# Kernel tuning notes

Hardware: AMD Instinct MI355X
Metric: run time of the kernel (lower is better)

## Reference

```python
import jax, jax.numpy as jnp
import numpy as np

B, S, D, H, W = 2, 8192, 512, 8, 256   # batch, seq, d_model, heads, one-sided window
HD = D // H                            # head dim = 64
C = S // W                             # number of chunks of size W (seq % 2W == 0 holds)


def setup_inputs() -> dict:
    key = jax.random.key(0)
    ks = jax.random.split(key, 7)
    x = jax.random.normal(ks[0], (B, S, D), jnp.float32)
    def w(k):
        return jax.random.normal(k, (D, D), jnp.float32) * 0.02
    def b(k):
        return jax.random.normal(k, (D,), jnp.float32) * 0.02
    return {
        "x": x,
        "Wq": w(ks[1]), "bq": b(ks[2]),
        "Wk": w(ks[3]), "bk": b(ks[4]),
        "Wv": w(ks[5]), "bv": b(ks[6]),
    }


def _heads_chunked(t):
    # (B,S,D) -> (B*H, C, W, HD): split heads, then split sequence into chunks of W
    return t.reshape(B, S, H, HD).transpose(0, 2, 1, 3).reshape(B * H, C, W, HD)


def _three_chunks(t):
    # neighbor-chunk concat: for chunk c, gather chunks [c-1, c, c+1] (zero padded at ends)
    tp = jnp.pad(t, ((0, 0), (1, 1), (0, 0), (0, 0)))
    return jnp.concatenate([tp[:, :-2], tp[:, 1:-1], tp[:, 2:]], axis=2)  # (B*H, C, 3W, HD)


def reference(x, Wq, bq, Wk, bk, Wv, bv):
    scale = 1.0 / np.sqrt(HD)
    q = _heads_chunked((x @ Wq + bq) * scale)
    k = _heads_chunked(x @ Wk + bk)
    v = _heads_chunked(x @ Wv + bv)

    k3 = _three_chunks(k)
    v3 = _three_chunks(v)

    # chunk-local scores against 3 neighboring chunks: (B*H, C, W, 3W)
    scores = jnp.einsum('bcxd,bcyd->bcxy', q, k3)

    # extract the (2W+1)-wide diagonal band: query x attends keys x..x+2W in the 3W window
    rows = jnp.arange(W)[:, None]                       # (W,1)
    diag = rows + jnp.arange(2 * W + 1)[None, :]        # (W, 2W+1) indices into 3W axis
    band = jnp.take_along_axis(scores, diag[None, None], axis=3)  # (B*H, C, W, 2W+1)

    # mask band entries whose global key position falls outside [0, S)
    pos = jnp.arange(S).reshape(C, W)[:, :, None] + (jnp.arange(2 * W + 1) - W)  # (C,W,2W+1)
    valid = (pos >= 0) & (pos < S)
    band = jnp.where(valid[None], band, -jnp.inf)

    probs = jax.nn.softmax(band, axis=-1)  # (B*H, C, W, 2W+1)

    # scatter band probs back into (W, 3W) layout and contract with values
    full = jnp.zeros((B * H, C, W, 3 * W), probs.dtype).at[:, :, rows, diag].set(probs)
    out = jnp.einsum('bcxy,bcyd->bcxd', full, v3)  # (B*H, C, W, HD)

    return out.reshape(B, H, S, HD).transpose(0, 2, 1, 3).reshape(B, S, D)
```

## Files before the change

### kernel.cpp

```cpp
#include <hip/hip_runtime.h>
#include <hip/hip_bf16.h>

#define S_LEN 8192
#define D_MODEL 512
#define NH 8
#define HD 64
#define WIN 256
#define NB 2

#define QSCALE 0.1803368801111204f

#define EXP2N(x) __builtin_amdgcn_exp2f(x)

typedef __hip_bfloat16 bf16;
typedef __attribute__((ext_vector_type(8))) short short8;
typedef __attribute__((ext_vector_type(4))) float f32x4;

static __device__ __forceinline__ short f2bf(float f) {
    bf16 h = __float2bfloat16(f);
    return *reinterpret_cast<short*>(&h);
}

static __device__ __forceinline__ void gload_lds16(short* lds, const short* g) {
    __builtin_amdgcn_global_load_lds(
        (const __attribute__((address_space(1))) void*)g,
        (__attribute__((address_space(3))) void*)lds, 16, 0, 0);
}

__global__ __launch_bounds__(256) void convert_x_kernel(
    const float* __restrict__ x, short* __restrict__ xb)
{
    const int n4 = (NB * S_LEN * D_MODEL) / 4;
    for (int i = blockIdx.x * 256 + threadIdx.x; i < n4; i += gridDim.x * 256) {
        float4 v = ((const float4*)x)[i];
        short4 o;
        o.x = f2bf(v.x); o.y = f2bf(v.y); o.z = f2bf(v.z); o.w = f2bf(v.w);
        ((short4*)xb)[i] = o;
    }
}

__global__ __launch_bounds__(256) void convert_wT_kernel(
    const float* __restrict__ Wq, const float* __restrict__ Wk,
    const float* __restrict__ Wv, short* __restrict__ wT)
{
    __shared__ float t[32][33];
    const float* W = blockIdx.z == 0 ? Wq : (blockIdx.z == 1 ? Wk : Wv);
    const int n0 = blockIdx.x * 32, k0 = blockIdx.y * 32;
    const int tx = threadIdx.x & 31, ty = threadIdx.x >> 5;
#pragma unroll
    for (int i = 0; i < 4; ++i)
        t[ty + 8 * i][tx] = W[(size_t)(k0 + ty + 8 * i) * D_MODEL + n0 + tx];
    __syncthreads();
#pragma unroll
    for (int i = 0; i < 4; ++i) {
        const int nl = ty + 8 * i, kl = tx;
        wT[(size_t)blockIdx.z * D_MODEL * D_MODEL +
           (size_t)(n0 + nl) * D_MODEL + k0 + kl] = f2bf(t[kl][nl]);
    }
}

__global__ __launch_bounds__(256) void proj_mfma_kernel(
    const short* __restrict__ xb, const short* __restrict__ wT,
    const float* __restrict__ bq, const float* __restrict__ bk,
    const float* __restrict__ bv, bf16* __restrict__ qkv)
{
    __shared__ short Ash[2][128 * 64];
    __shared__ short Bsh[2][128 * 64];

    const int nwg  = gridDim.x * gridDim.y;
    const int orig = blockIdx.y * gridDim.x + blockIdx.x;
    const int wid  = (orig & 7) * (nwg >> 3) + (orig >> 3);
    const int bx   = wid % 12;
    const int by   = wid / 12;

    const int widx = bx >> 2;
    const int col0 = (bx & 3) * 128;
    const int row0 = by * 128;
    const int tid  = threadIdx.x;
    const int w    = tid >> 6;
    const int lane = tid & 63;
    const int col  = lane & 15;
    const int kg   = lane >> 4;

    const float* bias = widx == 0 ? bq : (widx == 1 ? bk : bv);
    const float scale = widx == 0 ? QSCALE : 1.0f;
    const short* wbase = wT + (size_t)widx * D_MODEL * D_MODEL;

    const f32x4 zero4 = {0.f, 0.f, 0.f, 0.f};
    f32x4 acc[4][4];
#pragma unroll
    for (int i = 0; i < 4; ++i)
#pragma unroll
        for (int j = 0; j < 4; ++j) acc[i][j] = zero4;

    const int wm0 = (w >> 1) * 64;
    const int wn0 = (w & 1) * 64;

    auto stage = [&](int buf, int kb) {
#pragma unroll
        for (int ci = 0; ci < 4; ++ci) {
            const int Lb = w * 256 + ci * 64;
            const int L  = Lb + lane;
            const int mm = L >> 3;
            const int kc = ((L & 7) - (mm >> 1)) & 7;
            const int ko = kb + kc * 8;
            gload_lds16(&Ash[buf][Lb * 8],
                        xb + (size_t)(row0 + mm) * D_MODEL + ko);
            gload_lds16(&Bsh[buf][Lb * 8],
                        wbase + (size_t)(col0 + mm) * D_MODEL + ko);
        }
    };

    stage(0, 0);

    const int NSTEP = D_MODEL / 64;
    for (int it = 0; it < NSTEP; ++it) {
        __syncthreads();

        if (it + 1 < NSTEP) stage((it + 1) & 1, (it + 1) * 64);

        const short* Ab = Ash[it & 1];
        const short* Bb = Bsh[it & 1];

#pragma unroll
        for (int s = 0; s < 2; ++s) {
            short8 af[4], bfr[4];
#pragma unroll
            for (int mt = 0; mt < 4; ++mt) {
                const int m = wm0 + mt * 16 + col;
                const int c = m * 8 + ((s * 4 + kg + (m >> 1)) & 7);
                af[mt] = *(const short8*)(Ab + (size_t)c * 8);
            }
#pragma unroll
            for (int nt = 0; nt < 4; ++nt) {
                const int n = wn0 + nt * 16 + col;
                const int c = n * 8 + ((s * 4 + kg + (n >> 1)) & 7);
                bfr[nt] = *(const short8*)(Bb + (size_t)c * 8);
            }
#pragma unroll
            for (int mt = 0; mt < 4; ++mt)
#pragma unroll
                for (int nt = 0; nt < 4; ++nt)
                    acc[mt][nt] = __builtin_amdgcn_mfma_f32_16x16x32_bf16(
                        af[mt], bfr[nt], acc[mt][nt], 0, 0, 0);
        }
    }

    bf16* dst = qkv + (size_t)widx * (NB * NH * S_LEN * HD);
#pragma unroll
    for (int nt = 0; nt < 4; ++nt) {
        const int n = col0 + wn0 + nt * 16 + col;
        const float bias_v = bias[n];
        const int h = n >> 6, d = n & 63;
#pragma unroll
        for (int mt = 0; mt < 4; ++mt) {
            const int m0 = row0 + wm0 + mt * 16 + kg * 4;
            const int b = m0 >> 13, s0 = m0 & (S_LEN - 1);
            if (widx == 2) {
                short4 pk;
                pk.x = f2bf(acc[mt][nt][0] + bias_v);
                pk.y = f2bf(acc[mt][nt][1] + bias_v);
                pk.z = f2bf(acc[mt][nt][2] + bias_v);
                pk.w = f2bf(acc[mt][nt][3] + bias_v);
                *(short4*)&dst[(((size_t)(b * NH + h)) * HD + d) * S_LEN + s0] = pk;
            } else {
#pragma unroll
                for (int r = 0; r < 4; ++r)
                    dst[(((size_t)(b * NH + h)) * S_LEN + s0 + r) * HD + d] =
                        __float2bfloat16((acc[mt][nt][r] + bias_v) * scale);
            }
        }
    }
}

__global__ __launch_bounds__(256) void proj_kernel(
    const float* __restrict__ x, const float* __restrict__ Wm,
    const float* __restrict__ bias, bf16* __restrict__ dst, float scale,
    int transpose_v)
{
    __shared__ float As[16][64];
    __shared__ float Bs[16][64];
    const int tid  = threadIdx.x;
    const int row0 = blockIdx.y * 64;
    const int col0 = blockIdx.x * 64;
    const int ty = tid >> 4, tx = tid & 15;
    const int t4 = tid * 4;
    const int ai = t4 >> 4, aj = t4 & 15;
    const int bj = t4 >> 6, bi = t4 & 63;
    float acc[4][4] = {};
    for (int kb = 0; kb < D_MODEL; kb += 16) {
        float4 av = *(const float4*)(x  + (size_t)(row0 + ai) * D_MODEL + kb + aj);
        float4 bv = *(const float4*)(Wm + (size_t)(kb + bj)  * D_MODEL + col0 + bi);
        As[aj + 0][ai] = av.x; As[aj + 1][ai] = av.y;
        As[aj + 2][ai] = av.z; As[aj + 3][ai] = av.w;
        *(float4*)(&Bs[bj][bi]) = bv;
        __syncthreads();
#pragma unroll
        for (int k = 0; k < 16; ++k) {
            float a[4], b[4];
#pragma unroll
            for (int ii = 0; ii < 4; ++ii) a[ii] = As[k][ty * 4 + ii];
#pragma unroll
            for (int jj = 0; jj < 4; ++jj) b[jj] = Bs[k][tx * 4 + jj];
#pragma unroll
            for (int ii = 0; ii < 4; ++ii)
#pragma unroll
                for (int jj = 0; jj < 4; ++jj) acc[ii][jj] += a[ii] * b[jj];
        }
        __syncthreads();
    }
#pragma unroll
    for (int ii = 0; ii < 4; ++ii) {
        const int m = row0 + ty * 4 + ii;
        const int b = m >> 13, s = m & (S_LEN - 1);
#pragma unroll
        for (int jj = 0; jj < 4; ++jj) {
            const int n = col0 + tx * 4 + jj;
            const int h = n >> 6, d = n & 63;
            const float v = (acc[ii][jj] + bias[n]) * scale;
            if (transpose_v)
                dst[(((size_t)(b * NH + h)) * HD + d) * S_LEN + s] = __float2bfloat16(v);
            else
                dst[(((size_t)(b * NH + h)) * S_LEN + s) * HD + d] = __float2bfloat16(v);
        }
    }
}

__global__ __launch_bounds__(512) void attn_mfma5_kernel(
    const bf16* __restrict__ qw, const bf16* __restrict__ kw,
    const bf16* __restrict__ vt, float* __restrict__ out)
{
    __shared__ __align__(16) short Ksh[2][4096];
    __shared__ __align__(16) short Vsh[2][4096];
    __shared__ __align__(16) short Psh[8][16][72];

    const int orig = blockIdx.y * gridDim.x + blockIdx.x;
    const int wf   = (orig & 7) * 128 + (orig >> 3);
    const int bh   = wf >> 6;
    const int qt0  = (wf & 63) * 128;

    const int tid  = threadIdx.x;
    const int w    = tid >> 6;
    const int lane = tid & 63;
    const int col  = lane & 15;
    const int kg   = lane >> 4;
    const int q0   = qt0 + w * 16;
    const int q    = q0 + col;
    const size_t base = (size_t)bh * S_LEN * HD;

    const short* qg  = (const short*)qw;
    const short* kgp = (const short*)kw;
    const short* vgp = (const short*)vt;

    const int kt_lo = qt0 - WIN < 0 ? 0 : qt0 - WIN;
    const int kt_hi0 = qt0 + WIN + 64;
    const int kt_hi = kt_hi0 > S_LEN - 64 ? S_LEN - 64 : kt_hi0;
    const int NT    = ((kt_hi - kt_lo) >> 6) + 1;

    const int r0 = tid >> 3, c0 = (tid & 7) ^ (r0 & 7);
    const int ldsb = w * 64 * 8;

    const short* qptr = qg + base + (size_t)q * HD + kg * 8;
    const short8 qB0 = *(const short8*)(qptr);
    const short8 qB1 = *(const short8*)(qptr + 32);

    const f32x4 zero4 = {0.f, 0.f, 0.f, 0.f};
    f32x4 Oacc[4] = {zero4, zero4, zero4, zero4};
    float m = -1e30f, l = 0.f;

    const int x7 = col & 7;

    gload_lds16(&Ksh[0][ldsb], kgp + base + (size_t)(kt_lo + r0) * HD + c0 * 8);
    gload_lds16(&Vsh[0][ldsb], vgp + base + (size_t)r0 * S_LEN + kt_lo + c0 * 8);

    for (int i = 0; i < NT; ++i) {
        __syncthreads();

        if (i + 1 < NT) {
            const int ktn = kt_lo + 64 * (i + 1);
            const int nb = (i + 1) & 1;
            gload_lds16(&Ksh[nb][ldsb], kgp + base + (size_t)(ktn + r0) * HD + c0 * 8);
            gload_lds16(&Vsh[nb][ldsb], vgp + base + (size_t)r0 * S_LEN + ktn + c0 * 8);
        }

        const int kt = kt_lo + 64 * i;
        const short* Kb = Ksh[i & 1];
        const short* Vb = Vsh[i & 1];

        f32x4 sc[4];
        __builtin_amdgcn_s_setprio(1);
#pragma unroll
        for (int t = 0; t < 4; ++t) {
            const int key = 16 * t + col;
            const short8 kA0 = *(const short8*)(Kb + (size_t)(key * 8 + (kg ^ x7)) * 8);
            const short8 kA1 = *(const short8*)(Kb + (size_t)(key * 8 + ((kg + 4) ^ x7)) * 8);
            f32x4 a = zero4;
            a = __builtin_amdgcn_mfma_f32_16x16x32_bf16(kA0, qB0, a, 0, 0, 0);
            a = __builtin_amdgcn_mfma_f32_16x16x32_bf16(kA1, qB1, a, 0, 0, 0);
            sc[t] = a;
        }
        __builtin_amdgcn_s_setprio(0);

        const bool need_mask = (kt < q0 + 15 - WIN) || (kt + 63 > q0 + WIN);
        if (need_mask) {
#pragma unroll
            for (int t = 0; t < 4; ++t)
#pragma unroll
                for (int r = 0; r < 4; ++r) {
                    const int j = kt + 16 * t + kg * 4 + r;
                    if (j < q - WIN || j > q + WIN) sc[t][r] = -1e30f;
                }
        }

        float tm0 = fmaxf(fmaxf(sc[0][0], sc[0][1]), fmaxf(sc[0][2], sc[0][3]));
        float tm1 = fmaxf(fmaxf(sc[1][0], sc[1][1]), fmaxf(sc[1][2], sc[1][3]));
        float tm2 = fmaxf(fmaxf(sc[2][0], sc[2][1]), fmaxf(sc[2][2], sc[2][3]));
        float tm3 = fmaxf(fmaxf(sc[3][0], sc[3][1]), fmaxf(sc[3][2], sc[3][3]));
        float tmax = fmaxf(fmaxf(tm0, tm1), fmaxf(tm2, tm3));
        tmax = fmaxf(tmax, __shfl_xor(tmax, 16));
        tmax = fmaxf(tmax, __shfl_xor(tmax, 32));

        if (__any(tmax > m + 8.f)) {
            const float mnew = fmaxf(m, tmax);
            const float alpha = EXP2N(m - mnew);
            m = mnew;
#pragma unroll
            for (int dt = 0; dt < 4; ++dt)
#pragma unroll
                for (int r = 0; r < 4; ++r) Oacc[dt][r] *= alpha;
            l *= alpha;
        }

        float p[4][4];
#pragma unroll
        for (int t = 0; t < 4; ++t)
#pragma unroll
            for (int r = 0; r < 4; ++r) p[t][r] = EXP2N(sc[t][r] - m);

        float r0s = (p[0][0] + p[0][1]) + (p[0][2] + p[0][3]);
        float r1s = (p[1][0] + p[1][1]) + (p[1][2] + p[1][3]);
        float r2s = (p[2][0] + p[2][1]) + (p[2][2] + p[2][3]);
        float r3s = (p[3][0] + p[3][1]) + (p[3][2] + p[3][3]);
        float rs = (r0s + r1s) + (r2s + r3s);
        rs += __shfl_xor(rs, 16);
        rs += __shfl_xor(rs, 32);
        l += rs;

#pragma unroll
        for (int t = 0; t < 4; ++t) {
            short4 pk;
            pk.x = f2bf(p[t][0]); pk.y = f2bf(p[t][1]);
            pk.z = f2bf(p[t][2]); pk.w = f2bf(p[t][3]);
            *(short4*)&Psh[w][col][16 * t + 4 * kg] = pk;
        }

        const short* pp = &Psh[w][col][kg * 8];
        const short8 pB0 = *(const short8*)(pp);
        const short8 pB1 = *(const short8*)(pp + 32);

        __builtin_amdgcn_s_setprio(1);
#pragma unroll
        for (int dt = 0; dt < 4; ++dt) {
            const int d = dt * 16 + col;
            const short8 vA0 = *(const short8*)(Vb + (size_t)(d * 8 + (kg ^ x7)) * 8);
            const short8 vA1 = *(const short8*)(Vb + (size_t)(d * 8 + ((kg + 4) ^ x7)) * 8);
            Oacc[dt] = __builtin_amdgcn_mfma_f32_16x16x32_bf16(vA0, pB0, Oacc[dt], 0, 0, 0);
            Oacc[dt] = __builtin_amdgcn_mfma_f32_16x16x32_bf16(vA1, pB1, Oacc[dt], 0, 0, 0);
        }
        __builtin_amdgcn_s_setprio(0);
    }

    const float inv = 1.0f / l;
    const int b = bh >> 3, h = bh & 7;
    float* op = out + ((size_t)(b * S_LEN + q)) * D_MODEL + h * HD + kg * 4;
#pragma unroll
    for (int dt = 0; dt < 4; ++dt) {
        float4 o;
        o.x = Oacc[dt][0] * inv; o.y = Oacc[dt][1] * inv;
        o.z = Oacc[dt][2] * inv; o.w = Oacc[dt][3] * inv;
        *(float4*)(op + dt * 16) = o;
    }
}

extern "C" void kernel_launch(void* const* d_in, const int* in_sizes, int n_in,
                              void* d_out, int out_size, void* d_ws, size_t ws_size,
                              hipStream_t stream)
{
    const float* x  = (const float*)d_in[0];
    const float* Wq = (const float*)d_in[1];
    const float* bq = (const float*)d_in[2];
    const float* Wk = (const float*)d_in[3];
    const float* bk = (const float*)d_in[4];
    const float* Wv = (const float*)d_in[5];
    const float* bv = (const float*)d_in[6];
    float* out = (float*)d_out;

    const size_t n_elem = (size_t)NB * NH * S_LEN * HD;
    bf16* qw = (bf16*)d_ws;
    bf16* kw = qw + n_elem;
    bf16* vw = kw + n_elem;
    short* xb = (short*)(vw + n_elem);
    short* wT = xb + (size_t)NB * S_LEN * D_MODEL;

    const size_t need = (3 * n_elem + (size_t)NB * S_LEN * D_MODEL +
                         3 * (size_t)D_MODEL * D_MODEL) * sizeof(short);

    if (ws_size >= need) {
        convert_x_kernel<<<2048, 256, 0, stream>>>(x, xb);
        dim3 wgrid(D_MODEL / 32, D_MODEL / 32, 3);
        convert_wT_kernel<<<wgrid, 256, 0, stream>>>(Wq, Wk, Wv, wT);
        dim3 ggrid(12, (NB * S_LEN) / 128);
        proj_mfma_kernel<<<ggrid, 256, 0, stream>>>(xb, wT, bq, bk, bv, qw);
    } else {
        dim3 pgrid(D_MODEL / 64, (NB * S_LEN) / 64);
        proj_kernel<<<pgrid, 256, 0, stream>>>(x, Wq, bq, qw, QSCALE, 0);
        proj_kernel<<<pgrid, 256, 0, stream>>>(x, Wk, bk, kw, 1.0f, 0);
        proj_kernel<<<pgrid, 256, 0, stream>>>(x, Wv, bv, vw, 1.0f, 1);
    }

    dim3 agrid(NB * NH, S_LEN / 128);
    attn_mfma5_kernel<<<agrid, 512, 0, stream>>>(qw, kw, vw, out);
}
```

Measured before the change: 176.5 us.

## Fuse fp32-to-bf16 conversion of x into projection GEMM A-tile staging

Removes the separate kernel that converts x to bf16. The projection GEMM now loads fp32 x into registers, converts it, and writes it to LDS after the MFMA work of each step, in a register-prefetch pipeline. This saves one kernel launch and the round trip of writing and rereading a bf16 copy of x. In exchange, each GEMM tile reads twice as many bytes for A, and the extra registers and VALU conversion work may hurt occupancy.

```diff
diff --git a/kernel.cpp b/kernel.cpp
--- a/kernel.cpp
+++ b/kernel.cpp
@@ -25,18 +25,6 @@
     __builtin_amdgcn_global_load_lds(
         (const __attribute__((address_space(1))) void*)g,
         (__attribute__((address_space(3))) void*)lds, 16, 0, 0);
-}
-
-__global__ __launch_bounds__(256) void convert_x_kernel(
-    const float* __restrict__ x, short* __restrict__ xb)
-{
-    const int n4 = (NB * S_LEN * D_MODEL) / 4;
-    for (int i = blockIdx.x * 256 + threadIdx.x; i < n4; i += gridDim.x * 256) {
-        float4 v = ((const float4*)x)[i];
-        short4 o;
-        o.x = f2bf(v.x); o.y = f2bf(v.y); o.z = f2bf(v.z); o.w = f2bf(v.w);
-        ((short4*)xb)[i] = o;
-    }
 }
 
 __global__ __launch_bounds__(256) void convert_wT_kernel(
@@ -60,7 +48,7 @@
 }
 
 __global__ __launch_bounds__(256) void proj_mfma_kernel(
-    const short* __restrict__ xb, const short* __restrict__ wT,
+    const float* __restrict__ x, const short* __restrict__ wT,
     const float* __restrict__ bq, const float* __restrict__ bk,
     const float* __restrict__ bv, bf16* __restrict__ qkv)
 {
@@ -96,28 +84,57 @@
     const int wm0 = (w >> 1) * 64;
     const int wn0 = (w & 1) * 64;
 
-    auto stage = [&](int buf, int kb) {
+    auto stageB = [&](int buf, int kb) {
 #pragma unroll
         for (int ci = 0; ci < 4; ++ci) {
             const int Lb = w * 256 + ci * 64;
             const int L  = Lb + lane;
             const int mm = L >> 3;
             const int kc = ((L & 7) - (mm >> 1)) & 7;
-            const int ko = kb + kc * 8;
-            gload_lds16(&Ash[buf][Lb * 8],
-                        xb + (size_t)(row0 + mm) * D_MODEL + ko);
             gload_lds16(&Bsh[buf][Lb * 8],
-                        wbase + (size_t)(col0 + mm) * D_MODEL + ko);
+                        wbase + (size_t)(col0 + mm) * D_MODEL + kb + kc * 8);
         }
     };
 
-    stage(0, 0);
+    float4 ar[8];
+    auto loadA = [&](int kb) {
+#pragma unroll
+        for (int ci = 0; ci < 4; ++ci) {
+            const int L  = w * 256 + ci * 64 + lane;
+            const int mm = L >> 3;
+            const int kc = ((L & 7) - (mm >> 1)) & 7;
+            const float* src = x + (size_t)(row0 + mm) * D_MODEL + kb + kc * 8;
+            ar[2 * ci]     = *(const float4*)(src);
+            ar[2 * ci + 1] = *(const float4*)(src + 4);
+        }
+    };
+
+    auto writeA = [&](int buf) {
+#pragma unroll
+        for (int ci = 0; ci < 4; ++ci) {
+            const int L = w * 256 + ci * 64 + lane;
+            short8 s;
+            s[0] = f2bf(ar[2 * ci].x);     s[1] = f2bf(ar[2 * ci].y);
+            s[2] = f2bf(ar[2 * ci].z);     s[3] = f2bf(ar[2 * ci].w);
+            s[4] = f2bf(ar[2 * ci + 1].x); s[5] = f2bf(ar[2 * ci + 1].y);
+            s[6] = f2bf(ar[2 * ci + 1].z); s[7] = f2bf(ar[2 * ci + 1].w);
+            *(short8*)(&Ash[buf][(size_t)L * 8]) = s;
+        }
+    };
+
+    loadA(0);
+    stageB(0, 0);
+    writeA(0);
 
     const int NSTEP = D_MODEL / 64;
     for (int it = 0; it < NSTEP; ++it) {
         __syncthreads();
 
-        if (it + 1 < NSTEP) stage((it + 1) & 1, (it + 1) * 64);
+        const int nb = (it + 1) & 1;
+        if (it + 1 < NSTEP) {
+            stageB(nb, (it + 1) * 64);
+            loadA((it + 1) * 64);
+        }
 
         const short* Ab = Ash[it & 1];
         const short* Bb = Bsh[it & 1];
@@ -144,6 +161,8 @@
                     acc[mt][nt] = __builtin_amdgcn_mfma_f32_16x16x32_bf16(
                         af[mt], bfr[nt], acc[mt][nt], 0, 0, 0);
         }
+
+        if (it + 1 < NSTEP) writeA(nb);
     }
 
     bf16* dst = qkv + (size_t)widx * (NB * NH * S_LEN * HD);
@@ -399,18 +418,15 @@
     bf16* qw = (bf16*)d_ws;
     bf16* kw = qw + n_elem;
     bf16* vw = kw + n_elem;
-    short* xb = (short*)(vw + n_elem);
-    short* wT = xb + (size_t)NB * S_LEN * D_MODEL;
-
-    const size_t need = (3 * n_elem + (size_t)NB * S_LEN * D_MODEL +
-                         3 * (size_t)D_MODEL * D_MODEL) * sizeof(short);
+    short* wT = (short*)(vw + n_elem);
+
+    const size_t need = (3 * n_elem + 3 * (size_t)D_MODEL * D_MODEL) * sizeof(short);
 
     if (ws_size >= need) {
-        convert_x_kernel<<<2048, 256, 0, stream>>>(x, xb);
         dim3 wgrid(D_MODEL / 32, D_MODEL / 32, 3);
         convert_wT_kernel<<<wgrid, 256, 0, stream>>>(Wq, Wk, Wv, wT);
         dim3 ggrid(12, (NB * S_LEN) / 128);
-        proj_mfma_kernel<<<ggrid, 256, 0, stream>>>(xb, wT, bq, bk, bv, qw);
+        proj_mfma_kernel<<<ggrid, 256, 0, stream>>>(x, wT, bq, bk, bv, qw);
     } else {
         dim3 pgrid(D_MODEL / 64, (NB * S_LEN) / 64);
         proj_kernel<<<pgrid, 256, 0, stream>>>(x, Wq, bq, qw, QSCALE, 0);
```

New measurement: 189.3 us. +7.2%, slower.
